# Kernel tuning notes

Hardware: AMD Instinct MI355X
Metric: run time of the kernel (lower is better)

Reference implementation:

```python
import jax, jax.numpy as jnp
import numpy as np


def setup_inputs() -> dict:
    key = jax.random.key(0)
    k1, k2 = jax.random.split(key)
    pred = jax.random.normal(k1, (4, 8192, 3), dtype=jnp.float32)
    gt = jax.random.normal(k2, (4, 8192, 3), dtype=jnp.float32)
    return {"pred": pred, "gt": gt}


def reference(pred, gt):
    # pairwise squared distances: [B, N, M]
    diff = pred[:, :, None, :] - gt[:, None, :, :]
    distances = jnp.sum(diff ** 2, axis=-1)
    pred_to_gt = jnp.min(distances, axis=2)  # [B, N]
    gt_to_pred = jnp.min(distances, axis=1)  # [B, M]
    return jnp.mean(pred_to_gt) + jnp.mean(gt_to_pred)
```

## Files before the change

### kernel.cpp

```cpp
#include <hip/hip_runtime.h>
#include <math.h>


typedef _Float16 half8 __attribute__((ext_vector_type(8)));
typedef float f32x16 __attribute__((ext_vector_type(16)));

#define NPTS   8192
#define TT     512
#define NSPLIT 4
#define SCH    4
#define NQ_TOT 65536

__device__ __forceinline__ void split2(float v, _Float16& h, _Float16& l) {
  h = (_Float16)v; l = (_Float16)(v - (float)h);
}

__device__ __forceinline__ void pack_target(float x, float y, float z,
                                            half8& fa, half8& fb) {
  float s = x * x + y * y + z * z;
  _Float16 xh, xl, yh, yl, zh, zl, sh, sl;
  split2(x, xh, xl); split2(y, yh, yl); split2(z, zh, zl); split2(s, sh, sl);
  _Float16 one = (_Float16)1.0f;
  _Float16 Xh = (_Float16)(-2.f * (float)xh), Xl = (_Float16)(-2.f * (float)xl);
  _Float16 Yh = (_Float16)(-2.f * (float)yh), Yl = (_Float16)(-2.f * (float)yl);
  _Float16 Zh = (_Float16)(-2.f * (float)zh), Zl = (_Float16)(-2.f * (float)zl);
  fa = (half8){Xh, Xl, Xh, Xl, Yh, Yl, Yh, Yl};
  fb = (half8){Zh, Zl, Zh, Zl, sh, sl, one, one};
}

__global__ __launch_bounds__(256, 4) void chamfer_mfma(
    const float* __restrict__ pred, const float* __restrict__ gt,
    float* __restrict__ pmin, float* __restrict__ out) {
  __shared__ __align__(16) half8 lds[TT * 2];
  int bid = blockIdx.x;
  int split = bid & 3;
  int qblk  = (bid >> 2) & 31;
  int b     = (bid >> 7) & 3;
  int dir   = bid >> 9;
  const float* qsrc = dir ? gt : pred;
  const float* tsrc = dir ? pred : gt;
  int t = threadIdx.x, lane = t & 63, wave = t >> 6, ql = lane & 31;
  if (bid == 0 && t == 0) out[0] = 0.f;

  int qstart = qblk * 256 + wave * 64;
  const float* qb = qsrc + (size_t)(b * NPTS + qstart) * 3;
  float q0x = qb[3 * ql],        q0y = qb[3 * ql + 1],        q0z = qb[3 * ql + 2];
  float q1x = qb[3 * (ql + 32)], q1y = qb[3 * (ql + 32) + 1], q1z = qb[3 * (ql + 32) + 2];
  half8 bq0, bq1;
  {
    float s0 = q0x * q0x + q0y * q0y + q0z * q0z;
    float s1 = q1x * q1x + q1y * q1y + q1z * q1z;
    _Float16 x0h, x0l, y0h, y0l, z0h, z0l, s0h, s0l;
    _Float16 x1h, x1l, y1h, y1l, z1h, z1l, s1h, s1l;
    split2(q0x, x0h, x0l); split2(q0y, y0h, y0l); split2(q0z, z0h, z0l); split2(s0, s0h, s0l);
    split2(q1x, x1h, x1l); split2(q1y, y1h, y1l); split2(q1z, z1h, z1l); split2(s1, s1h, s1l);
    _Float16 one = (_Float16)1.0f;
    bq0 = (lane < 32) ? (half8){x0h, x0h, x0l, x0l, y0h, y0h, y0l, y0l}
                      : (half8){z0h, z0h, z0l, z0l, one, one, s0h, s0l};
    bq1 = (lane < 32) ? (half8){x1h, x1h, x1l, x1l, y1h, y1h, y1l, y1l}
                      : (half8){z1h, z1h, z1l, z1l, one, one, s1h, s1l};
  }

  const float* tb = tsrc + (size_t)(b * NPTS + split * (SCH * TT)) * 3;
  float p0x, p0y, p0z, p1x, p1y, p1z;
  {
    const float* s0 = tb + (size_t)t * 3;
    const float* s1 = tb + (size_t)(t + 256) * 3;
    p0x = s0[0]; p0y = s0[1]; p0z = s0[2];
    p1x = s1[0]; p1y = s1[1]; p1z = s1[2];
  }

  float vacc0[8], vacc1[8];
  #pragma unroll
  for (int j = 0; j < 8; ++j) { vacc0[j] = INFINITY; vacc1[j] = INFINITY; }

  f32x16 zero = {};
  for (int tc = 0; tc < SCH; ++tc) {
    half8 f0a, f0b, f1a, f1b;
    pack_target(p0x, p0y, p0z, f0a, f0b);
    pack_target(p1x, p1y, p1z, f1a, f1b);
    if (tc) __syncthreads();
    int base0 = (t >> 5) * 64 + (t & 31);
    lds[base0]            = f0a;
    lds[base0 + 32]       = f0b;
    lds[base0 + 512]      = f1a;
    lds[base0 + 512 + 32] = f1b;
    if (tc + 1 < SCH) {
      const float* s0 = tb + (size_t)((tc + 1) * TT + t) * 3;
      const float* s1 = tb + (size_t)((tc + 1) * TT + t + 256) * 3;
      p0x = s0[0]; p0y = s0[1]; p0z = s0[2];
      p1x = s1[0]; p1y = s1[1]; p1z = s1[2];
    }
    __syncthreads();
    #pragma unroll 2
    for (int g = 0; g < TT / 32; ++g) {
      half8 a = lds[g * 64 + lane];
      f32x16 d0 = __builtin_amdgcn_mfma_f32_32x32x16_f16(a, bq0, zero, 0, 0, 0);
      f32x16 d1 = __builtin_amdgcn_mfma_f32_32x32x16_f16(a, bq1, zero, 0, 0, 0);
      #pragma unroll
      for (int j = 0; j < 8; ++j) {
        vacc0[j] = fminf(fminf(vacc0[j], d0[2 * j]), d0[2 * j + 1]);
        vacc1[j] = fminf(fminf(vacc1[j], d1[2 * j]), d1[2 * j + 1]);
      }
    }
  }
  float a0 = fminf(fminf(vacc0[0], vacc0[1]), vacc0[2]);
  float a1 = fminf(fminf(vacc0[3], vacc0[4]), vacc0[5]);
  float a2 = fminf(vacc0[6], vacc0[7]);
  float m0 = fminf(fminf(a0, a1), a2);
  float b0 = fminf(fminf(vacc1[0], vacc1[1]), vacc1[2]);
  float b1 = fminf(fminf(vacc1[3], vacc1[4]), vacc1[5]);
  float b2 = fminf(vacc1[6], vacc1[7]);
  float m1 = fminf(fminf(b0, b1), b2);
  m0 = fminf(m0, __shfl_xor(m0, 32, 64));
  m1 = fminf(m1, __shfl_xor(m1, 32, 64));

  if (lane < 32) {
    size_t qi = (size_t)dir * 32768 + (size_t)b * NPTS + qstart + ql;
    pmin[(size_t)split * NQ_TOT + qi]      = m0;
    pmin[(size_t)split * NQ_TOT + qi + 32] = m1;
  }
}

__global__ __launch_bounds__(256) void reduce_kernel(
    const float* __restrict__ pmin, float* __restrict__ out) {
  __shared__ float wsum[4];
  float acc = 0.f;
  for (int i = blockIdx.x * 256 + threadIdx.x; i < NQ_TOT; i += 64 * 256) {
    float v = pmin[i];
    #pragma unroll
    for (int s = 1; s < NSPLIT; ++s) v = fminf(v, pmin[(size_t)s * NQ_TOT + i]);
    acc += fmaxf(v, 0.f);
  }
  acc *= (1.0f / 32768.0f);
  #pragma unroll
  for (int off = 32; off > 0; off >>= 1) acc += __shfl_down(acc, off, 64);
  int wid = threadIdx.x >> 6;
  if ((threadIdx.x & 63) == 0) wsum[wid] = acc;
  __syncthreads();
  if (threadIdx.x == 0) atomicAdd(out, wsum[0] + wsum[1] + wsum[2] + wsum[3]);
}

extern "C" void kernel_launch(void* const* d_in, const int* in_sizes, int n_in,
                              void* d_out, int out_size, void* d_ws, size_t ws_size,
                              hipStream_t stream) {
  const float* pred = (const float*)d_in[0];
  const float* gt   = (const float*)d_in[1];
  float* out = (float*)d_out;
  float* pmin = (float*)d_ws;

  chamfer_mfma<<<1024, 256, 0, stream>>>(pred, gt, pmin, out);
  reduce_kernel<<<64, 256, 0, stream>>>(pmin, out);
}
```

Baseline: 73.87 us.

## Process four query tiles per wave and split targets into eight chunks

Each wave now holds four query fragments (128 queries) instead of two, so every LDS target fragment read feeds four MFMAs instead of two. The target range is split eight ways with two chunks each, which keeps the grid at 1024 blocks and cuts per-block staging and sync steps. Empty asm barriers on the MFMA results stop the compiler from interleaving them, which helps bound register pressure. The costs are more VGPRs for the extra accumulators, which could hurt occupancy under the 4-blocks bound, and twice as many partial minima for the reduce kernel to read.

```diff
diff --git a/kernel.cpp b/kernel.cpp
--- a/kernel.cpp
+++ b/kernel.cpp
@@ -7,8 +7,8 @@
 
 #define NPTS   8192
 #define TT     512
-#define NSPLIT 4
-#define SCH    4
+#define NSPLIT 8
+#define SCH    2
 #define NQ_TOT 65536
 
 __device__ __forceinline__ void split2(float v, _Float16& h, _Float16& l) {
@@ -28,37 +28,39 @@
   fb = (half8){Zh, Zl, Zh, Zl, sh, sl, one, one};
 }
 
+__device__ __forceinline__ half8 pack_query(float x, float y, float z, bool lo) {
+  float s = x * x + y * y + z * z;
+  _Float16 xh, xl, yh, yl, zh, zl, sh, sl;
+  split2(x, xh, xl); split2(y, yh, yl); split2(z, zh, zl); split2(s, sh, sl);
+  _Float16 one = (_Float16)1.0f;
+  return lo ? (half8){xh, xh, xl, xl, yh, yh, yl, yl}
+            : (half8){zh, zh, zl, zl, one, one, sh, sl};
+}
+
 __global__ __launch_bounds__(256, 4) void chamfer_mfma(
     const float* __restrict__ pred, const float* __restrict__ gt,
     float* __restrict__ pmin, float* __restrict__ out) {
   __shared__ __align__(16) half8 lds[TT * 2];
   int bid = blockIdx.x;
-  int split = bid & 3;
-  int qblk  = (bid >> 2) & 31;
+  int split = bid & 7;
+  int qblk  = (bid >> 3) & 15;
   int b     = (bid >> 7) & 3;
   int dir   = bid >> 9;
   const float* qsrc = dir ? gt : pred;
   const float* tsrc = dir ? pred : gt;
   int t = threadIdx.x, lane = t & 63, wave = t >> 6, ql = lane & 31;
+  bool lo = (lane < 32);
   if (bid == 0 && t == 0) out[0] = 0.f;
 
-  int qstart = qblk * 256 + wave * 64;
+  int qstart = qblk * 512 + wave * 128;
   const float* qb = qsrc + (size_t)(b * NPTS + qstart) * 3;
-  float q0x = qb[3 * ql],        q0y = qb[3 * ql + 1],        q0z = qb[3 * ql + 2];
-  float q1x = qb[3 * (ql + 32)], q1y = qb[3 * (ql + 32) + 1], q1z = qb[3 * (ql + 32) + 2];
-  half8 bq0, bq1;
+  half8 bq0, bq1, bq2, bq3;
   {
-    float s0 = q0x * q0x + q0y * q0y + q0z * q0z;
-    float s1 = q1x * q1x + q1y * q1y + q1z * q1z;
-    _Float16 x0h, x0l, y0h, y0l, z0h, z0l, s0h, s0l;
-    _Float16 x1h, x1l, y1h, y1l, z1h, z1l, s1h, s1l;
-    split2(q0x, x0h, x0l); split2(q0y, y0h, y0l); split2(q0z, z0h, z0l); split2(s0, s0h, s0l);
-    split2(q1x, x1h, x1l); split2(q1y, y1h, y1l); split2(q1z, z1h, z1l); split2(s1, s1h, s1l);
-    _Float16 one = (_Float16)1.0f;
-    bq0 = (lane < 32) ? (half8){x0h, x0h, x0l, x0l, y0h, y0h, y0l, y0l}
-                      : (half8){z0h, z0h, z0l, z0l, one, one, s0h, s0l};
-    bq1 = (lane < 32) ? (half8){x1h, x1h, x1l, x1l, y1h, y1h, y1l, y1l}
-                      : (half8){z1h, z1h, z1l, z1l, one, one, s1h, s1l};
+    int i0 = 3 * ql, i1 = 3 * (ql + 32), i2 = 3 * (ql + 64), i3 = 3 * (ql + 96);
+    bq0 = pack_query(qb[i0], qb[i0 + 1], qb[i0 + 2], lo);
+    bq1 = pack_query(qb[i1], qb[i1 + 1], qb[i1 + 2], lo);
+    bq2 = pack_query(qb[i2], qb[i2 + 1], qb[i2 + 2], lo);
+    bq3 = pack_query(qb[i3], qb[i3 + 1], qb[i3 + 2], lo);
   }
 
   const float* tb = tsrc + (size_t)(b * NPTS + split * (SCH * TT)) * 3;
@@ -70,9 +72,12 @@
     p1x = s1[0]; p1y = s1[1]; p1z = s1[2];
   }
 
-  float vacc0[8], vacc1[8];
+  float vacc0[8], vacc1[8], vacc2[8], vacc3[8];
   #pragma unroll
-  for (int j = 0; j < 8; ++j) { vacc0[j] = INFINITY; vacc1[j] = INFINITY; }
+  for (int j = 0; j < 8; ++j) {
+    vacc0[j] = INFINITY; vacc1[j] = INFINITY;
+    vacc2[j] = INFINITY; vacc3[j] = INFINITY;
+  }
 
   f32x16 zero = {};
   for (int tc = 0; tc < SCH; ++tc) {
@@ -92,33 +97,55 @@
       p1x = s1[0]; p1y = s1[1]; p1z = s1[2];
     }
     __syncthreads();
+
     #pragma unroll 2
     for (int g = 0; g < TT / 32; ++g) {
       half8 a = lds[g * 64 + lane];
       f32x16 d0 = __builtin_amdgcn_mfma_f32_32x32x16_f16(a, bq0, zero, 0, 0, 0);
       f32x16 d1 = __builtin_amdgcn_mfma_f32_32x32x16_f16(a, bq1, zero, 0, 0, 0);
+      asm("" : "+v"(d0), "+v"(d1));
       #pragma unroll
       for (int j = 0; j < 8; ++j) {
         vacc0[j] = fminf(fminf(vacc0[j], d0[2 * j]), d0[2 * j + 1]);
         vacc1[j] = fminf(fminf(vacc1[j], d1[2 * j]), d1[2 * j + 1]);
       }
+      f32x16 d2 = __builtin_amdgcn_mfma_f32_32x32x16_f16(a, bq2, zero, 0, 0, 0);
+      f32x16 d3 = __builtin_amdgcn_mfma_f32_32x32x16_f16(a, bq3, zero, 0, 0, 0);
+      asm("" : "+v"(d2), "+v"(d3));
+      #pragma unroll
+      for (int j = 0; j < 8; ++j) {
+        vacc2[j] = fminf(fminf(vacc2[j], d2[2 * j]), d2[2 * j + 1]);
+        vacc3[j] = fminf(fminf(vacc3[j], d3[2 * j]), d3[2 * j + 1]);
+      }
     }
   }
-  float a0 = fminf(fminf(vacc0[0], vacc0[1]), vacc0[2]);
-  float a1 = fminf(fminf(vacc0[3], vacc0[4]), vacc0[5]);
-  float a2 = fminf(vacc0[6], vacc0[7]);
-  float m0 = fminf(fminf(a0, a1), a2);
-  float b0 = fminf(fminf(vacc1[0], vacc1[1]), vacc1[2]);
-  float b1 = fminf(fminf(vacc1[3], vacc1[4]), vacc1[5]);
-  float b2 = fminf(vacc1[6], vacc1[7]);
-  float m1 = fminf(fminf(b0, b1), b2);
+  float m0, m1, m2, m3;
+  {
+    float a0 = fminf(fminf(vacc0[0], vacc0[1]), fminf(vacc0[2], vacc0[3]));
+    float a1 = fminf(fminf(vacc0[4], vacc0[5]), fminf(vacc0[6], vacc0[7]));
+    m0 = fminf(a0, a1);
+    float b0 = fminf(fminf(vacc1[0], vacc1[1]), fminf(vacc1[2], vacc1[3]));
+    float b1 = fminf(fminf(vacc1[4], vacc1[5]), fminf(vacc1[6], vacc1[7]));
+    m1 = fminf(b0, b1);
+    float c0 = fminf(fminf(vacc2[0], vacc2[1]), fminf(vacc2[2], vacc2[3]));
+    float c1 = fminf(fminf(vacc2[4], vacc2[5]), fminf(vacc2[6], vacc2[7]));
+    m2 = fminf(c0, c1);
+    float e0 = fminf(fminf(vacc3[0], vacc3[1]), fminf(vacc3[2], vacc3[3]));
+    float e1 = fminf(fminf(vacc3[4], vacc3[5]), fminf(vacc3[6], vacc3[7]));
+    m3 = fminf(e0, e1);
+  }
   m0 = fminf(m0, __shfl_xor(m0, 32, 64));
   m1 = fminf(m1, __shfl_xor(m1, 32, 64));
+  m2 = fminf(m2, __shfl_xor(m2, 32, 64));
+  m3 = fminf(m3, __shfl_xor(m3, 32, 64));
 
   if (lane < 32) {
     size_t qi = (size_t)dir * 32768 + (size_t)b * NPTS + qstart + ql;
-    pmin[(size_t)split * NQ_TOT + qi]      = m0;
-    pmin[(size_t)split * NQ_TOT + qi + 32] = m1;
+    float* p = pmin + (size_t)split * NQ_TOT + qi;
+    p[0]  = m0;
+    p[32] = m1;
+    p[64] = m2;
+    p[96] = m3;
   }
 }
 
```

Result: slower. 76.28 us (+3.3%).
